# Performance work log

Measured on AMD Instinct MI355X. Metric: run time of the kernel, lower is better.

Reference implementation:

```python
import jax, jax.numpy as jnp
import numpy as np

TOPK = 2
ALPHA_AUX = 0.02

def setup_inputs() -> dict:
    key = jax.random.key(0)
    ks = jax.random.split(key, 6)
    B, T, D, E, H = 2, 2048, 1024, 16, 1536
    s_in = 1.0 / np.sqrt(D)
    s_h = 1.0 / np.sqrt(H)
    return {
        "x": jax.random.normal(ks[0], (B, T, D), dtype=jnp.float32),
        "router_w": jax.random.normal(ks[1], (E, D), dtype=jnp.float32) * s_in,
        "w1": jax.random.normal(ks[2], (E, H, D), dtype=jnp.float32) * s_in,
        "b1": jax.random.normal(ks[3], (E, H), dtype=jnp.float32) * 0.01,
        "w2": jax.random.normal(ks[4], (E, D, H), dtype=jnp.float32) * s_h,
        "b2": jax.random.normal(ks[5], (E, D), dtype=jnp.float32) * 0.01,
    }

def reference(x, router_w, w1, b1, w2, b2):
    B, T, D = x.shape
    E = router_w.shape[0]
    N = B * T
    x_flat = x.reshape(N, D)

    # Router: top-k logits -> softmax gates -> dense dispatch matrix [N, E]
    logits = x_flat @ router_w.T                      # [N, E]
    vals, idx = jax.lax.top_k(logits, TOPK)           # [N, K]
    gate = jax.nn.softmax(vals, axis=-1)              # [N, K]
    rows = jnp.arange(N)[:, None]
    dispatch = jnp.zeros((N, E), dtype=x.dtype).at[rows, idx].set(gate)

    # Expert MLPs computed densely over all experts; gate==0 masks unselected,
    # reproducing the gather-MLP-scatter math exactly.
    h = jnp.einsum('nd,ehd->neh', x_flat, w1) + b1    # [N, E, H]
    h = jax.nn.gelu(h, approximate=True)              # tanh GELU
    y = jnp.einsum('neh,edh->ned', h, w2) + b2        # [N, E, D]
    out = jnp.einsum('ne,ned->nd', dispatch, y).reshape(B, T, D)

    # Auxiliary load-balancing loss
    tok_per_expert = (dispatch > 0).sum(0).astype(jnp.float32)  # [E]
    f_i = tok_per_expert / tok_per_expert.sum()
    m_i = dispatch.sum(0) / jnp.clip(tok_per_expert, 1.0, None)
    aux_loss = ALPHA_AUX * (f_i * m_i).mean()
    return out, aux_loss
```

## Files before the change

kernel.cpp:

```cpp
#include <hip/hip_runtime.h>
#include <hip/hip_bf16.h>
#include <math.h>

#define N_TOK 4096
#define DIM   1024
#define NEXP  16
#define HID   1536
#define TOPK2 2
#define NASSIGN (N_TOK * TOPK2)

#define MAX_ITEMS 80
#define G1_BLOCKS (MAX_ITEMS * 12)
#define W_ELEMS   (NEXP * HID * DIM)
#define CVT_BLOCKS (W_ELEMS / 4 / 256)

typedef __attribute__((ext_vector_type(8))) short short8;
typedef __attribute__((ext_vector_type(4))) float floatx4;
typedef unsigned short u16;

#define GLOAD_LDS16(gp, lp)                                                     \
    __builtin_amdgcn_global_load_lds(                                           \
        (const __attribute__((address_space(1))) unsigned int*)(gp),            \
        (__attribute__((address_space(3))) unsigned int*)(lp), 16, 0, 0)

__device__ __forceinline__ void cvt_one4(const float* __restrict__ src,
                                         u16* __restrict__ dst, int i) {
    float4 v = ((const float4*)src)[i];
    __hip_bfloat16 a = __float2bfloat16(v.x), b = __float2bfloat16(v.y);
    __hip_bfloat16 c = __float2bfloat16(v.z), d = __float2bfloat16(v.w);
    ushort4 o;
    o.x = *(u16*)&a; o.y = *(u16*)&b; o.z = *(u16*)&c; o.w = *(u16*)&d;
    ((ushort4*)dst)[i] = o;
}

__global__ void cvt_kernel(const float* __restrict__ src, u16* __restrict__ dst, int n4) {
    int i = blockIdx.x * 256 + threadIdx.x;
    if (i >= n4) return;
    cvt_one4(src, dst, i);
}

__global__ __launch_bounds__(256)
void router_cvtw1_kernel(const float* __restrict__ x, const float* __restrict__ rw,
                         int* __restrict__ idx, float* __restrict__ gate,
                         u16* __restrict__ x_bf,
                         const float* __restrict__ w1src, u16* __restrict__ w1dst) {
    int tid = threadIdx.x;
    if (blockIdx.x >= 256) {
        int i = (blockIdx.x - 256) * 256 + tid;
        cvt_one4(w1src, w1dst, i);
        return;
    }
    int tb = blockIdx.x * 16;
    __shared__ float xs[16][68];
    __shared__ float rs[16][68];
    __shared__ float lg[16][17];

    int t = tid >> 4, e = tid & 15;
    int srow = tid >> 4, scol = (tid & 15) * 4;

    float acc = 0.f;
    for (int k0 = 0; k0 < DIM; k0 += 64) {
        float4 xv = *(const float4*)&x[(size_t)(tb + srow) * DIM + k0 + scol];
        *(float4*)&xs[srow][scol] = xv;
        *(float4*)&rs[srow][scol] = *(const float4*)&rw[(size_t)srow * DIM + k0 + scol];
        {
            __hip_bfloat16 a = __float2bfloat16(xv.x), b = __float2bfloat16(xv.y);
            __hip_bfloat16 c = __float2bfloat16(xv.z), d = __float2bfloat16(xv.w);
            ushort4 o;
            o.x = *(u16*)&a; o.y = *(u16*)&b; o.z = *(u16*)&c; o.w = *(u16*)&d;
            *(ushort4*)&x_bf[(size_t)(tb + srow) * DIM + k0 + scol] = o;
        }
        __syncthreads();
        const float2* xp = (const float2*)xs[t];
        const float2* rp = (const float2*)rs[e];
        #pragma unroll
        for (int k = 0; k < 32; k++) {
            float2 a = xp[k], b = rp[k];
            acc = fmaf(a.x, b.x, acc);
            acc = fmaf(a.y, b.y, acc);
        }
        __syncthreads();
    }
    lg[t][e] = acc;
    __syncthreads();

    if (tid < 16) {
        int n = tb + tid;
        float v0 = -3.402823466e+38f, v1 = -3.402823466e+38f;
        int i0 = 0, i1 = 0;
        #pragma unroll
        for (int ee = 0; ee < NEXP; ee++) {
            float v = lg[tid][ee];
            if (v > v0) { v1 = v0; i1 = i0; v0 = v; i0 = ee; }
            else if (v > v1) { v1 = v; i1 = ee; }
        }
        float e1 = expf(v1 - v0);
        float inv = 1.f / (1.f + e1);
        idx[2 * n] = i0; idx[2 * n + 1] = i1;
        gate[2 * n] = inv; gate[2 * n + 1] = e1 * inv;
    }
}

__global__ __launch_bounds__(256)
void plan_kernel(const int* __restrict__ idx, const float* __restrict__ gate,
                 int* __restrict__ offsets, int* __restrict__ tlist,
                 int* __restrict__ slot_of,
                 int* __restrict__ wl, int* __restrict__ wcount,
                 float* __restrict__ aux_out) {
    __shared__ int cnt_s[16];
    __shared__ float gs_s[16];
    __shared__ int pos_s[16];
    __shared__ int offs_s[17];
    int tid = threadIdx.x;
    if (tid < 16) { cnt_s[tid] = 0; gs_s[tid] = 0.f; pos_s[tid] = 0; }
    __syncthreads();
    for (int i = tid; i < NASSIGN; i += 256) {
        int e = idx[i];
        atomicAdd(&cnt_s[e], 1);
        atomicAdd(&gs_s[e], gate[i]);
    }
    __syncthreads();
    if (tid == 0) {
        int acc = 0;
        for (int e = 0; e < NEXP; e++) { offs_s[e] = acc; acc += cnt_s[e]; }
        offs_s[NEXP] = acc;
        float tot = (float)acc;
        float s = 0.f;
        for (int e = 0; e < NEXP; e++) {
            float c = (float)cnt_s[e];
            s += (c / tot) * (gs_s[e] / fmaxf(c, 1.f));
        }
        *aux_out = 0.02f * (s / (float)NEXP);
        int m = 0;
        for (int e = 0; e < NEXP; e++) {
            int nt = (cnt_s[e] + 127) >> 7;
            for (int rt = 0; rt < nt; rt++) wl[m++] = (e << 8) | rt;
        }
        *wcount = m;
    }
    __syncthreads();
    if (tid < 17) offsets[tid] = offs_s[tid];
    for (int i = tid; i < NASSIGN; i += 256) {
        int e = idx[i];
        int p = atomicAdd(&pos_s[e], 1);
        int s = offs_s[e] + p;
        tlist[s] = i;
        slot_of[i] = s;
    }
}

__device__ __forceinline__ float gelu_tanh(float v) {
    float v3 = v * v * v;
    float t = tanhf(0.7978845608028654f * (v + 0.044715f * v3));
    return 0.5f * v * (1.f + t);
}


__global__ __launch_bounds__(256)
void gemm1_cvtw2_kernel(const u16* __restrict__ xb, const u16* __restrict__ w1b,
                        const float* __restrict__ b1,
                        const int* __restrict__ offsets, const int* __restrict__ tlist,
                        const int* __restrict__ wl, const int* __restrict__ wcount,
                        u16* __restrict__ h_bf,
                        const float* __restrict__ w2src, u16* __restrict__ w2dst) {
    int bid = blockIdx.x;
    int tid = threadIdx.x;
    if (bid >= G1_BLOCKS) {
        int i = (bid - G1_BLOCKS) * 256 + tid;
        cvt_one4(w2src, w2dst, i);
        return;
    }
    int item = bid / 12;
    if (item >= *wcount) return;
    int colt = bid - item * 12;
    int w = wl[item];
    int e = w >> 8, rt = w & 255;
    int beg = offsets[e], ne = offsets[e + 1] - beg;
    int row0 = rt * 128, col0 = colt * 128;

    __shared__ u16 As[2][128 * 32];
    __shared__ u16 Bs[2][128 * 32];

    int wave = tid >> 6, lane = tid & 63;
    int wm = wave & 1, wn = wave >> 1;

    int koff = (((lane & 3) ^ ((lane >> 3) & 3)) * 8);
    const u16* aptr[2];
    const u16* bptr[2];
    #pragma unroll
    for (int q = 0; q < 2; q++) {
        int lrow = wave * 32 + q * 16 + (lane >> 2);
        int gi = beg + row0 + lrow;
        int gi2 = (row0 + lrow < ne) ? gi : beg;
        int tok = tlist[gi2] >> 1;
        aptr[q] = xb + (size_t)tok * DIM + koff;
        int n = col0 + lrow;
        bptr[q] = w1b + (size_t)(e * HID + n) * DIM + koff;
    }

    int rchunk = (((lane >> 4) ^ ((lane >> 1) & 3)) * 8);

    floatx4 acc[4][4] = {};
    #pragma unroll
    for (int q = 0; q < 2; q++) {
        GLOAD_LDS16(aptr[q], &As[0][(wave * 32 + q * 16) * 32]);
        GLOAD_LDS16(bptr[q], &Bs[0][(wave * 32 + q * 16) * 32]);
    }
    __syncthreads();
    int cur = 0;
    for (int k0 = 0; k0 < DIM; k0 += 32) {
        if (k0 + 32 < DIM) {
            #pragma unroll
            for (int q = 0; q < 2; q++) {
                GLOAD_LDS16(aptr[q] + k0 + 32, &As[cur ^ 1][(wave * 32 + q * 16) * 32]);
                GLOAD_LDS16(bptr[q] + k0 + 32, &Bs[cur ^ 1][(wave * 32 + q * 16) * 32]);
            }
        }
        short8 af[4], bf_[4];
        #pragma unroll
        for (int mi = 0; mi < 4; mi++)
            af[mi] = *(const short8*)&As[cur][(wm * 64 + mi * 16 + (lane & 15)) * 32 + rchunk];
        #pragma unroll
        for (int nj = 0; nj < 4; nj++)
            bf_[nj] = *(const short8*)&Bs[cur][(wn * 64 + nj * 16 + (lane & 15)) * 32 + rchunk];
        #pragma unroll
        for (int mi = 0; mi < 4; mi++)
            #pragma unroll
            for (int nj = 0; nj < 4; nj++)
                acc[mi][nj] = __builtin_amdgcn_mfma_f32_16x16x32_bf16(af[mi], bf_[nj], acc[mi][nj], 0, 0, 0);
        __syncthreads();
        cur ^= 1;
    }

    #pragma unroll
    for (int mi = 0; mi < 4; mi++) {
        #pragma unroll
        for (int r = 0; r < 4; r++) {
            int lrow = wm * 64 + mi * 16 + (lane >> 4) * 4 + r;
            if (row0 + lrow >= ne) continue;
            size_t orow = (size_t)(beg + row0 + lrow);
            #pragma unroll
            for (int nj = 0; nj < 4; nj++) {
                int col = col0 + wn * 64 + nj * 16 + (lane & 15);
                float v = acc[mi][nj][r] + b1[e * HID + col];
                __hip_bfloat16 hb = __float2bfloat16(gelu_tanh(v));
                h_bf[orow * HID + col] = *(u16*)&hb;
            }
        }
    }
}

__global__ __launch_bounds__(256)
void gemm2_kernel(const u16* __restrict__ h_bf, const u16* __restrict__ w2b,
                  const float* __restrict__ b2,
                  const int* __restrict__ offsets, const int* __restrict__ tlist,
                  const int* __restrict__ wl, const int* __restrict__ wcount,
                  const float* __restrict__ gate, float* __restrict__ ydst,
                  int use_y) {
    int bid = blockIdx.x;
    int item = bid >> 3;
    if (item >= *wcount) return;
    int colt = bid & 7;
    int w = wl[item];
    int e = w >> 8, rt = w & 255;
    int beg = offsets[e], ne = offsets[e + 1] - beg;
    int row0 = rt * 128, col0 = colt * 128;

    __shared__ u16 As[2][128 * 32];
    __shared__ u16 Bs[2][128 * 32];

    int tid = threadIdx.x;
    int wave = tid >> 6, lane = tid & 63;
    int wm = wave & 1, wn = wave >> 1;

    int koff = (((lane & 3) ^ ((lane >> 3) & 3)) * 8);
    const u16* aptr[2];
    const u16* bptr[2];
    #pragma unroll
    for (int q = 0; q < 2; q++) {
        int lrow = wave * 32 + q * 16 + (lane >> 2);
        int gi = beg + row0 + lrow;
        int gi2 = (row0 + lrow < ne) ? gi : beg;
        aptr[q] = h_bf + (size_t)gi2 * HID + koff;
        int n = col0 + lrow;
        bptr[q] = w2b + (size_t)(e * DIM + n) * HID + koff;
    }

    int rchunk = (((lane >> 4) ^ ((lane >> 1) & 3)) * 8);

    floatx4 acc[4][4] = {};
    #pragma unroll
    for (int q = 0; q < 2; q++) {
        GLOAD_LDS16(aptr[q], &As[0][(wave * 32 + q * 16) * 32]);
        GLOAD_LDS16(bptr[q], &Bs[0][(wave * 32 + q * 16) * 32]);
    }
    __syncthreads();
    int cur = 0;
    for (int k0 = 0; k0 < HID; k0 += 32) {
        if (k0 + 32 < HID) {
            #pragma unroll
            for (int q = 0; q < 2; q++) {
                GLOAD_LDS16(aptr[q] + k0 + 32, &As[cur ^ 1][(wave * 32 + q * 16) * 32]);
                GLOAD_LDS16(bptr[q] + k0 + 32, &Bs[cur ^ 1][(wave * 32 + q * 16) * 32]);
            }
        }
        short8 af[4], bf_[4];
        #pragma unroll
        for (int mi = 0; mi < 4; mi++)
            af[mi] = *(const short8*)&As[cur][(wm * 64 + mi * 16 + (lane & 15)) * 32 + rchunk];
        #pragma unroll
        for (int nj = 0; nj < 4; nj++)
            bf_[nj] = *(const short8*)&Bs[cur][(wn * 64 + nj * 16 + (lane & 15)) * 32 + rchunk];
        #pragma unroll
        for (int mi = 0; mi < 4; mi++)
            #pragma unroll
            for (int nj = 0; nj < 4; nj++)
                acc[mi][nj] = __builtin_amdgcn_mfma_f32_16x16x32_bf16(af[mi], bf_[nj], acc[mi][nj], 0, 0, 0);
        __syncthreads();
        cur ^= 1;
    }

    #pragma unroll
    for (int mi = 0; mi < 4; mi++) {
        #pragma unroll
        for (int r = 0; r < 4; r++) {
            int lrow = wm * 64 + mi * 16 + (lane >> 4) * 4 + r;
            if (row0 + lrow >= ne) continue;
            int slot = beg + row0 + lrow;
            int t = tlist[slot];
            float g = gate[t];
            if (use_y) {
                #pragma unroll
                for (int nj = 0; nj < 4; nj++) {
                    int col = col0 + wn * 64 + nj * 16 + (lane & 15);
                    float v = g * (acc[mi][nj][r] + b2[e * DIM + col]);
                    ydst[(size_t)slot * DIM + col] = v;
                }
            } else {
                int tok = t >> 1;
                #pragma unroll
                for (int nj = 0; nj < 4; nj++) {
                    int col = col0 + wn * 64 + nj * 16 + (lane & 15);
                    float v = g * (acc[mi][nj][r] + b2[e * DIM + col]);
                    atomicAdd(&ydst[(size_t)tok * DIM + col], v);
                }
            }
        }
    }
}

__global__ __launch_bounds__(256)
void combine_kernel(const float* __restrict__ y, const int* __restrict__ slot_of,
                    float* __restrict__ out) {
    int t = blockIdx.x;
    int c4 = threadIdx.x;
    int s0 = slot_of[2 * t], s1 = slot_of[2 * t + 1];
    float4 a = ((const float4*)(y + (size_t)s0 * DIM))[c4];
    float4 b = ((const float4*)(y + (size_t)s1 * DIM))[c4];
    float4 o;
    o.x = a.x + b.x; o.y = a.y + b.y; o.z = a.z + b.z; o.w = a.w + b.w;
    ((float4*)(out + (size_t)t * DIM))[c4] = o;
}

extern "C" void kernel_launch(void* const* d_in, const int* in_sizes, int n_in,
                              void* d_out, int out_size, void* d_ws, size_t ws_size,
                              hipStream_t stream) {
    const float* x  = (const float*)d_in[0];
    const float* rw = (const float*)d_in[1];
    const float* w1 = (const float*)d_in[2];
    const float* b1 = (const float*)d_in[3];
    const float* w2 = (const float*)d_in[4];
    const float* b2 = (const float*)d_in[5];
    float* out = (float*)d_out;

    char* ws = (char*)d_ws;
    int*   offsets = (int*)(ws + 192);
    int*   wcount  = (int*)(ws + 384);
    int*   wl      = (int*)(ws + 512);
    int*   idx     = (int*)(ws + 4096);
    float* gate    = (float*)(ws + 4096 + 4 * NASSIGN);
    int*   tlist   = (int*)(ws + 4096 + 8 * NASSIGN);
    int*   slot_of = (int*)(ws + 4096 + 12 * NASSIGN);
    u16*   x_bf    = (u16*)(ws + (256 << 10));
    u16*   h_bf    = x_bf + (size_t)N_TOK * DIM;
    u16*   w1_bf   = h_bf + (size_t)NASSIGN * HID;
    u16*   w2_bf   = w1_bf + (size_t)W_ELEMS;

    const size_t NEED_FULL = (size_t)(256 << 10)
                           + (size_t)N_TOK * DIM * 2
                           + (size_t)NASSIGN * HID * 2
                           + (size_t)W_ELEMS * 2 * 2;
    int full = (ws_size >= NEED_FULL) ? 1 : 0;

    if (full) {
        float* y = (float*)w1_bf;

        router_cvtw1_kernel<<<256 + CVT_BLOCKS, 256, 0, stream>>>(
            x, rw, idx, gate, x_bf, w1, w1_bf);
        plan_kernel<<<1, 256, 0, stream>>>(idx, gate, offsets, tlist, slot_of,
                                           wl, wcount, out + (size_t)N_TOK * DIM);
        gemm1_cvtw2_kernel<<<G1_BLOCKS + CVT_BLOCKS, 256, 0, stream>>>(
            x_bf, w1_bf, b1, offsets, tlist, wl, wcount, h_bf, w2, w2_bf);
        gemm2_kernel<<<MAX_ITEMS * 8, 256, 0, stream>>>(
            h_bf, w2_bf, b2, offsets, tlist, wl, wcount, gate, y, 1);
        combine_kernel<<<N_TOK, 256, 0, stream>>>(y, slot_of, out);
    } else {
        u16* w_bf = w1_bf;
        hipMemsetAsync(d_out, 0, (size_t)out_size * 4, stream);
        router_cvtw1_kernel<<<256 + CVT_BLOCKS, 256, 0, stream>>>(
            x, rw, idx, gate, x_bf, w1, w_bf);
        plan_kernel<<<1, 256, 0, stream>>>(idx, gate, offsets, tlist, slot_of,
                                           wl, wcount, out + (size_t)N_TOK * DIM);
        gemm1_cvtw2_kernel<<<G1_BLOCKS, 256, 0, stream>>>(
            x_bf, w_bf, b1, offsets, tlist, wl, wcount, h_bf, w2, w_bf);
        cvt_kernel<<<CVT_BLOCKS, 256, 0, stream>>>(w2, w_bf, W_ELEMS / 4);
        gemm2_kernel<<<MAX_ITEMS * 8, 256, 0, stream>>>(
            h_bf, w_bf, b2, offsets, tlist, wl, wcount, gate, out, 0);
    }
}
```

Baseline: 402.7 us.

## Triple-buffer LDS in expert GEMMs with explicit vmcnt waits

Both expert GEMM kernels move from a double-buffered LDS pipeline to a three-stage ring. Two k-tiles are kept in flight, and partial s_waitcnt vmcnt plus raw barriers replace __syncthreads. The aim is to hide global-to-LDS load latency behind MFMA work instead of stalling on every tile. In exchange LDS use rises by half (48KB per block), which may lower occupancy, and the hand-counted vmcnt values must match the four loads issued per stage.

```diff
diff --git a/kernel.cpp b/kernel.cpp
--- a/kernel.cpp
+++ b/kernel.cpp
@@ -22,6 +22,12 @@
     __builtin_amdgcn_global_load_lds(                                           \
         (const __attribute__((address_space(1))) unsigned int*)(gp),            \
         (__attribute__((address_space(3))) unsigned int*)(lp), 16, 0, 0)
+
+#define WAITV(N) do {                                              \
+    asm volatile("s_waitcnt vmcnt(" #N ")" ::: "memory");          \
+    __builtin_amdgcn_sched_barrier(0);                             \
+} while (0)
+#define BARRIER_RAW() __builtin_amdgcn_s_barrier()
 
 __device__ __forceinline__ void cvt_one4(const float* __restrict__ src,
                                          u16* __restrict__ dst, int i) {
@@ -178,8 +184,8 @@
     int beg = offsets[e], ne = offsets[e + 1] - beg;
     int row0 = rt * 128, col0 = colt * 128;
 
-    __shared__ u16 As[2][128 * 32];
-    __shared__ u16 Bs[2][128 * 32];
+    __shared__ u16 As[3][128 * 32];
+    __shared__ u16 Bs[3][128 * 32];
 
     int wave = tid >> 6, lane = tid & 63;
     int wm = wave & 1, wn = wave >> 1;
@@ -201,35 +207,41 @@
     int rchunk = (((lane >> 4) ^ ((lane >> 1) & 3)) * 8);
 
     floatx4 acc[4][4] = {};
-    #pragma unroll
-    for (int q = 0; q < 2; q++) {
-        GLOAD_LDS16(aptr[q], &As[0][(wave * 32 + q * 16) * 32]);
-        GLOAD_LDS16(bptr[q], &Bs[0][(wave * 32 + q * 16) * 32]);
-    }
-    __syncthreads();
-    int cur = 0;
-    for (int k0 = 0; k0 < DIM; k0 += 32) {
-        if (k0 + 32 < DIM) {
-            #pragma unroll
-            for (int q = 0; q < 2; q++) {
-                GLOAD_LDS16(aptr[q] + k0 + 32, &As[cur ^ 1][(wave * 32 + q * 16) * 32]);
-                GLOAD_LDS16(bptr[q] + k0 + 32, &Bs[cur ^ 1][(wave * 32 + q * 16) * 32]);
-            }
-        }
+
+    auto STAGE = [&](int kt, int b) {
+        #pragma unroll
+        for (int q = 0; q < 2; q++) {
+            GLOAD_LDS16(aptr[q] + kt * 32, &As[b][(wave * 32 + q * 16) * 32]);
+            GLOAD_LDS16(bptr[q] + kt * 32, &Bs[b][(wave * 32 + q * 16) * 32]);
+        }
+    };
+    auto CONSUME = [&](int b) {
         short8 af[4], bf_[4];
         #pragma unroll
         for (int mi = 0; mi < 4; mi++)
-            af[mi] = *(const short8*)&As[cur][(wm * 64 + mi * 16 + (lane & 15)) * 32 + rchunk];
+            af[mi] = *(const short8*)&As[b][(wm * 64 + mi * 16 + (lane & 15)) * 32 + rchunk];
         #pragma unroll
         for (int nj = 0; nj < 4; nj++)
-            bf_[nj] = *(const short8*)&Bs[cur][(wn * 64 + nj * 16 + (lane & 15)) * 32 + rchunk];
+            bf_[nj] = *(const short8*)&Bs[b][(wn * 64 + nj * 16 + (lane & 15)) * 32 + rchunk];
         #pragma unroll
         for (int mi = 0; mi < 4; mi++)
             #pragma unroll
             for (int nj = 0; nj < 4; nj++)
                 acc[mi][nj] = __builtin_amdgcn_mfma_f32_16x16x32_bf16(af[mi], bf_[nj], acc[mi][nj], 0, 0, 0);
-        __syncthreads();
-        cur ^= 1;
+    };
+
+    const int NT = DIM / 32;
+    STAGE(0, 0); STAGE(1, 1);
+    int bc = 0, bn = 1, bs = 2;
+    for (int t = 0; t < NT; ++t) {
+        if (t + 2 < NT)      { STAGE(t + 2, bs); WAITV(8); }
+        else if (t + 1 < NT) { WAITV(4); }
+        else                 { WAITV(0); }
+        BARRIER_RAW();
+        CONSUME(bc);
+        __builtin_amdgcn_sched_barrier(0);
+        BARRIER_RAW();
+        int tmp = bc; bc = bn; bn = bs; bs = tmp;
     }
 
     #pragma unroll
@@ -266,8 +278,8 @@
     int beg = offsets[e], ne = offsets[e + 1] - beg;
     int row0 = rt * 128, col0 = colt * 128;
 
-    __shared__ u16 As[2][128 * 32];
-    __shared__ u16 Bs[2][128 * 32];
+    __shared__ u16 As[3][128 * 32];
+    __shared__ u16 Bs[3][128 * 32];
 
     int tid = threadIdx.x;
     int wave = tid >> 6, lane = tid & 63;
@@ -289,35 +301,41 @@
     int rchunk = (((lane >> 4) ^ ((lane >> 1) & 3)) * 8);
 
     floatx4 acc[4][4] = {};
-    #pragma unroll
-    for (int q = 0; q < 2; q++) {
-        GLOAD_LDS16(aptr[q], &As[0][(wave * 32 + q * 16) * 32]);
-        GLOAD_LDS16(bptr[q], &Bs[0][(wave * 32 + q * 16) * 32]);
-    }
-    __syncthreads();
-    int cur = 0;
-    for (int k0 = 0; k0 < HID; k0 += 32) {
-        if (k0 + 32 < HID) {
-            #pragma unroll
-            for (int q = 0; q < 2; q++) {
-                GLOAD_LDS16(aptr[q] + k0 + 32, &As[cur ^ 1][(wave * 32 + q * 16) * 32]);
-                GLOAD_LDS16(bptr[q] + k0 + 32, &Bs[cur ^ 1][(wave * 32 + q * 16) * 32]);
-            }
-        }
+
+    auto STAGE = [&](int kt, int b) {
+        #pragma unroll
+        for (int q = 0; q < 2; q++) {
+            GLOAD_LDS16(aptr[q] + kt * 32, &As[b][(wave * 32 + q * 16) * 32]);
+            GLOAD_LDS16(bptr[q] + kt * 32, &Bs[b][(wave * 32 + q * 16) * 32]);
+        }
+    };
+    auto CONSUME = [&](int b) {
         short8 af[4], bf_[4];
         #pragma unroll
         for (int mi = 0; mi < 4; mi++)
-            af[mi] = *(const short8*)&As[cur][(wm * 64 + mi * 16 + (lane & 15)) * 32 + rchunk];
+            af[mi] = *(const short8*)&As[b][(wm * 64 + mi * 16 + (lane & 15)) * 32 + rchunk];
         #pragma unroll
         for (int nj = 0; nj < 4; nj++)
-            bf_[nj] = *(const short8*)&Bs[cur][(wn * 64 + nj * 16 + (lane & 15)) * 32 + rchunk];
+            bf_[nj] = *(const short8*)&Bs[b][(wn * 64 + nj * 16 + (lane & 15)) * 32 + rchunk];
         #pragma unroll
         for (int mi = 0; mi < 4; mi++)
             #pragma unroll
             for (int nj = 0; nj < 4; nj++)
                 acc[mi][nj] = __builtin_amdgcn_mfma_f32_16x16x32_bf16(af[mi], bf_[nj], acc[mi][nj], 0, 0, 0);
-        __syncthreads();
-        cur ^= 1;
+    };
+
+    const int NT = HID / 32;
+    STAGE(0, 0); STAGE(1, 1);
+    int bc = 0, bn = 1, bs = 2;
+    for (int t = 0; t < NT; ++t) {
+        if (t + 2 < NT)      { STAGE(t + 2, bs); WAITV(8); }
+        else if (t + 1 < NT) { WAITV(4); }
+        else                 { WAITV(0); }
+        BARRIER_RAW();
+        CONSUME(bc);
+        __builtin_amdgcn_sched_barrier(0);
+        BARRIER_RAW();
+        int tmp = bc; bc = bn; bn = bs; bs = tmp;
     }
 
     #pragma unroll
```

Result: no change. 397.7 us (-1.3%).
